# Kernel optimization log

Hardware: AMD Instinct MI355X
Metric: run time of the kernel (lower is better)

## Reference

```python
import jax, jax.numpy as jnp
import numpy as np
from jax import lax

NUM_HEADS = 4
DIM = 192
EPS = 1e-12  # torch F.normalize eps


def setup_inputs() -> dict:
    key = jax.random.key(0)
    ks = jax.random.split(key, 5)
    b, c, h, w = 8, DIM, 128, 128
    x = jax.random.normal(ks[0], (b, c, h, w), dtype=jnp.float32)
    f = jax.random.normal(ks[1], (b, c, h, w), dtype=jnp.float32)
    # conv weights, scaled like kaiming-ish init
    w_qkv = jax.random.normal(ks[2], (3 * c, c, 1, 1), dtype=jnp.float32) * (1.0 / np.sqrt(c))
    w_dw = jax.random.normal(ks[3], (3 * c, 1, 3, 3), dtype=jnp.float32) * (1.0 / 3.0)
    w_proj = jax.random.normal(ks[4], (c, c, 1, 1), dtype=jnp.float32) * (1.0 / np.sqrt(c))
    temperature = jnp.ones((NUM_HEADS, 1, 1), dtype=jnp.float32)
    return {"x": x, "f": f, "w_qkv": w_qkv, "w_dw": w_dw, "w_proj": w_proj,
            "temperature": temperature}


def _conv(x, w, groups=1):
    return lax.conv_general_dilated(
        x, w, window_strides=(1, 1), padding="SAME",
        dimension_numbers=("NCHW", "OIHW", "NCHW"),
        feature_group_count=groups)


def reference(x, f, w_qkv, w_dw, w_proj, temperature):
    b, c, h, w = x.shape
    x_in = x + f
    qkv = _conv(x_in, w_qkv)                 # [b, 3c, h, w] 1x1 conv
    qkv = _conv(qkv, w_dw, groups=3 * c)     # depthwise 3x3
    q, k, v = jnp.split(qkv, 3, axis=1)      # each [b, c, h, w]
    hw = h * w
    ch = c // NUM_HEADS

    def heads(t):
        return t.reshape(b, NUM_HEADS, ch, hw)  # 'b (head c) h w -> b head c (h w)'

    q, k, v = heads(q), heads(k), heads(v)
    # L2-normalize over spatial (last) dim, torch-style eps clamp
    q = q / jnp.maximum(jnp.linalg.norm(q, axis=-1, keepdims=True), EPS)
    k = k / jnp.maximum(jnp.linalg.norm(k, axis=-1, keepdims=True), EPS)
    # transposed (channel) attention: [b, head, ch, ch]
    attn = jnp.einsum("bhcn,bhdn->bhcd", q, k) * temperature[None]
    attn = jax.nn.softmax(attn, axis=-1)
    out = jnp.einsum("bhcd,bhdn->bhcn", attn, v)  # [b, head, ch, hw]
    out = out.reshape(b, c, h, w)
    return _conv(out, w_proj)
```

## Files before the change

### kernel.cpp

```cpp
#include <hip/hip_runtime.h>
#include <stdint.h>

#define NB 8
#define NC 192
#define NOC 576
#define NH 4
#define HW 16384
#define NCHUNK 16

typedef unsigned short u16;
typedef __bf16 v8bf __attribute__((ext_vector_type(8)));
typedef float v4f __attribute__((ext_vector_type(4)));
typedef u16 v8us __attribute__((ext_vector_type(8)));
typedef u16 v4us __attribute__((ext_vector_type(4)));

__device__ __forceinline__ u16 f2bf(float f) {
    uint32_t u = __float_as_uint(f);
    u += 0x7FFFu + ((u >> 16) & 1u);
    return (u16)(u >> 16);
}
__device__ __forceinline__ float bf2f(u16 u) {
    return __uint_as_float(((uint32_t)u) << 16);
}

__global__ void k_cvt_w(const float* __restrict__ w, u16* __restrict__ wb, int n) {
    int i = blockIdx.x * 256 + threadIdx.x;
    if (i < n) wb[i] = f2bf(w[i]);
}

__global__ __launch_bounds__(256, 2) void k_gemm_qkv(
    const float* __restrict__ x, const float* __restrict__ f,
    const u16* __restrict__ wb, u16* __restrict__ qkv, int b0)
{
    __shared__ u16 bt[64 * 192];
    const int t = threadIdx.x;
    const int bl = blockIdx.y;
    const int bg = b0 + bl;
    const int p0 = blockIdx.x * 64;

    {
        const int qp = t & 15;
        const int chw = t >> 4;
        const int px = qp * 4;
        #pragma unroll
        for (int pass = 0; pass < 12; ++pass) {
            const int ch = pass * 16 + chw;
            const size_t base = ((size_t)bg * NC + ch) * HW + p0 + px;
            const float4 xv = *reinterpret_cast<const float4*>(&x[base]);
            const float4 fv = *reinterpret_cast<const float4*>(&f[base]);
            const int c4 = ch >> 3, cl = ch & 7;
            bt[(px + 0) * 192 + ((c4 ^ ((px + 0) & 7)) << 3) + cl] = f2bf(xv.x + fv.x);
            bt[(px + 1) * 192 + ((c4 ^ ((px + 1) & 7)) << 3) + cl] = f2bf(xv.y + fv.y);
            bt[(px + 2) * 192 + ((c4 ^ ((px + 2) & 7)) << 3) + cl] = f2bf(xv.z + fv.z);
            bt[(px + 3) * 192 + ((c4 ^ ((px + 3) & 7)) << 3) + cl] = f2bf(xv.w + fv.w);
        }
    }
    __syncthreads();

    const int w = t >> 6, l = t & 63, lr = l & 15, lg = l >> 4;
    const int oc0 = w * 144;

    v4f acc[4][9];
    #pragma unroll
    for (int mi = 0; mi < 4; ++mi)
        #pragma unroll
        for (int ni = 0; ni < 9; ++ni)
            acc[mi][ni] = (v4f){0.f, 0.f, 0.f, 0.f};

    #pragma unroll
    for (int ks = 0; ks < 6; ++ks) {
        const int k = ks * 32 + lg * 8;
        const int c4 = ks * 4 + lg;
        v8bf a[4];
        #pragma unroll
        for (int mi = 0; mi < 4; ++mi) {
            const int px = mi * 16 + lr;
            a[mi] = *reinterpret_cast<const v8bf*>(&bt[px * 192 + ((c4 ^ (px & 7)) << 3)]);
        }
        #pragma unroll
        for (int ni = 0; ni < 9; ++ni) {
            const int oc = oc0 + ni * 16 + lr;
            const v8bf bw = *reinterpret_cast<const v8bf*>(&wb[oc * 192 + k]);
            #pragma unroll
            for (int mi = 0; mi < 4; ++mi)
                acc[mi][ni] = __builtin_amdgcn_mfma_f32_16x16x32_bf16(a[mi], bw, acc[mi][ni], 0, 0, 0);
        }
    }

    #pragma unroll
    for (int mi = 0; mi < 4; ++mi)
        #pragma unroll
        for (int ni = 0; ni < 9; ++ni) {
            const int oc = oc0 + ni * 16 + lr;
            const int px = p0 + mi * 16 + lg * 4;
            v4us pk;
            pk[0] = f2bf(acc[mi][ni][0]); pk[1] = f2bf(acc[mi][ni][1]);
            pk[2] = f2bf(acc[mi][ni][2]); pk[3] = f2bf(acc[mi][ni][3]);
            *reinterpret_cast<v4us*>(&qkv[((size_t)bl * NOC + oc) * HW + px]) = pk;
        }
}

__global__ __launch_bounds__(256) void k_dw(
    const u16* __restrict__ qkv, const float* __restrict__ wdw,
    u16* __restrict__ qk_out, u16* __restrict__ v_out,
    float* __restrict__ sumsq, int b0)
{
    __shared__ u16 plane[128 * 136];
    __shared__ float red[4];
    const int t = threadIdx.x;
    const int ch = blockIdx.x;
    const int bl = blockIdx.y;
    const int bg = b0 + bl;
    const size_t pbase = ((size_t)bl * NOC + ch) * HW;

    float wk[9];
    #pragma unroll
    for (int i = 0; i < 9; ++i) wk[i] = wdw[ch * 9 + i];

    const int r = t >> 1;
    const int cb = (t & 1) * 64;

    #pragma unroll
    for (int i = 0; i < 8; ++i) {
        v8us v = *reinterpret_cast<const v8us*>(&qkv[pbase + r * 128 + cb + i * 8]);
        *reinterpret_cast<v8us*>(&plane[r * 136 + cb + i * 8]) = v;
    }
    __syncthreads();

    const bool vm = (r > 0), vp = (r < 127);
    const u16* rowm = &plane[(r - 1) * 136];
    const u16* rowc = &plane[r * 136];
    const u16* rowp = &plane[(r + 1) * 136];

    float am, ac, bm, bc, cm, cc2;
    if (cb == 0) { am = 0.f; bm = 0.f; cm = 0.f; }
    else {
        am = vm ? bf2f(rowm[cb - 1]) : 0.f;
        bm = bf2f(rowc[cb - 1]);
        cm = vp ? bf2f(rowp[cb - 1]) : 0.f;
    }
    ac = vm ? bf2f(rowm[cb]) : 0.f;
    bc = bf2f(rowc[cb]);
    cc2 = vp ? bf2f(rowp[cb]) : 0.f;

    uint32_t ov[32];
    float ssq = 0.f;
    #pragma unroll
    for (int xp = 0; xp < 32; ++xp) {
        #pragma unroll
        for (int s2 = 0; s2 < 2; ++s2) {
            const int col = cb + xp * 2 + s2;
            float ap, bp, cp;
            if (col < 127) {
                ap = vm ? bf2f(rowm[col + 1]) : 0.f;
                bp = bf2f(rowc[col + 1]);
                cp = vp ? bf2f(rowp[col + 1]) : 0.f;
            } else { ap = 0.f; bp = 0.f; cp = 0.f; }
            float o = wk[0]*am + wk[1]*ac + wk[2]*ap
                    + wk[3]*bm + wk[4]*bc + wk[5]*bp
                    + wk[6]*cm + wk[7]*cc2 + wk[8]*cp;
            u16 ob = f2bf(o);
            float orr = bf2f(ob);
            ssq += orr * orr;
            ov[xp] = (s2 == 0) ? (uint32_t)ob : (ov[xp] | ((uint32_t)ob << 16));
            am = ac; ac = ap; bm = bc; bc = bp; cm = cc2; cc2 = cp;
        }
    }

    __syncthreads();
    #pragma unroll
    for (int i = 0; i < 32; ++i)
        *reinterpret_cast<uint32_t*>(&plane[r * 136 + cb + i * 2]) = ov[i];
    __syncthreads();

    u16* dst = (ch < 2 * NC) ? (qk_out + ((size_t)bg * (2 * NC) + ch) * HW)
                             : (v_out + ((size_t)bg * NC + (ch - 2 * NC)) * HW);
    #pragma unroll
    for (int i = 0; i < 8; ++i) {
        const int idx = i * 2048 + t * 8;
        const int rr = idx >> 7, cc = idx & 127;
        v8us v = *reinterpret_cast<const v8us*>(&plane[rr * 136 + cc]);
        *reinterpret_cast<v8us*>(&dst[idx]) = v;
    }

    #pragma unroll
    for (int off = 32; off > 0; off >>= 1) ssq += __shfl_down(ssq, off);
    if ((t & 63) == 0) red[t >> 6] = ssq;
    __syncthreads();
    if (t == 0 && ch < 2 * NC) sumsq[bg * (2 * NC) + ch] = red[0] + red[1] + red[2] + red[3];
}

__global__ __launch_bounds__(256) void k_attn(
    const u16* __restrict__ qk, float* __restrict__ partials)
{
    __shared__ float wsum[4 * 2304];
    const int t = threadIdx.x;
    const int chunk = blockIdx.x;
    const int h = blockIdx.y;
    const int b = blockIdx.z;
    const int w = t >> 6, l = t & 63, lr = l & 15, lg = l >> 4;

    const size_t qbase = ((size_t)b * 384 + h * 48) * HW;
    const size_t kbase = ((size_t)b * 384 + 192 + h * 48) * HW;
    const int pb = chunk * 1024 + w * 256;

    v4f acc[3][3];
    #pragma unroll
    for (int mi = 0; mi < 3; ++mi)
        #pragma unroll
        for (int ni = 0; ni < 3; ++ni)
            acc[mi][ni] = (v4f){0.f, 0.f, 0.f, 0.f};

    #pragma unroll
    for (int ks = 0; ks < 8; ++ks) {
        const int k = pb + ks * 32 + lg * 8;
        v8bf a[3], bb[3];
        #pragma unroll
        for (int mi = 0; mi < 3; ++mi)
            a[mi] = *reinterpret_cast<const v8bf*>(&qk[qbase + (size_t)(mi * 16 + lr) * HW + k]);
        #pragma unroll
        for (int ni = 0; ni < 3; ++ni)
            bb[ni] = *reinterpret_cast<const v8bf*>(&qk[kbase + (size_t)(ni * 16 + lr) * HW + k]);
        #pragma unroll
        for (int mi = 0; mi < 3; ++mi)
            #pragma unroll
            for (int ni = 0; ni < 3; ++ni)
                acc[mi][ni] = __builtin_amdgcn_mfma_f32_16x16x32_bf16(a[mi], bb[ni], acc[mi][ni], 0, 0, 0);
    }

    #pragma unroll
    for (int mi = 0; mi < 3; ++mi)
        #pragma unroll
        for (int ni = 0; ni < 3; ++ni)
            #pragma unroll
            for (int r = 0; r < 4; ++r)
                wsum[w * 2304 + (mi * 16 + lg * 4 + r) * 48 + ni * 16 + lr] = acc[mi][ni][r];
    __syncthreads();

    #pragma unroll
    for (int i = 0; i < 9; ++i) {
        const int e = t + i * 256;
        float s = wsum[e] + wsum[2304 + e] + wsum[4608 + e] + wsum[6912 + e];
        partials[(((size_t)(b * NH + h)) * NCHUNK + chunk) * 2304 + e] = s;
    }
}

__global__ __launch_bounds__(256) void k_smx(
    const float* __restrict__ partials, const float* __restrict__ sumsq,
    const float* __restrict__ wproj, const float* __restrict__ temp,
    u16* __restrict__ Mb)
{
    __shared__ float att[2304];
    __shared__ float rq[48], rk[48];
    const int t = threadIdx.x;
    const int h = blockIdx.x;
    const int b = blockIdx.y;

    if (t < 48) {
        float s = sumsq[b * 384 + h * 48 + t];
        rq[t] = 1.f / fmaxf(sqrtf(s), 1e-12f);
    } else if (t < 96) {
        float s = sumsq[b * 384 + 192 + h * 48 + (t - 48)];
        rk[t - 48] = 1.f / fmaxf(sqrtf(s), 1e-12f);
    }
    __syncthreads();
    const float tp = temp[h];
    #pragma unroll
    for (int i = 0; i < 9; ++i) {
        const int e = t + i * 256;
        const float* pp = &partials[(((size_t)(b * NH + h)) * NCHUNK) * 2304 + e];
        float s = 0.f;
        #pragma unroll
        for (int c = 0; c < NCHUNK; ++c) s += pp[(size_t)c * 2304];
        att[e] = s * rq[e / 48] * rk[e % 48] * tp;
    }
    __syncthreads();
    if (t < 48) {
        float m = -1e30f;
        #pragma unroll
        for (int j = 0; j < 48; ++j) m = fmaxf(m, att[t * 48 + j]);
        float s = 0.f;
        for (int j = 0; j < 48; ++j) { float e2 = __expf(att[t * 48 + j] - m); att[t * 48 + j] = e2; s += e2; }
        const float inv = 1.f / s;
        for (int j = 0; j < 48; ++j) att[t * 48 + j] *= inv;
    }
    __syncthreads();
    #pragma unroll
    for (int i = 0; i < 36; ++i) {
        const int idx = t + i * 256;
        const int oc = idx / 48, d = idx % 48;
        float s = 0.f;
        #pragma unroll
        for (int cc = 0; cc < 48; ++cc)
            s += wproj[oc * 192 + h * 48 + cc] * att[cc * 48 + d];
        Mb[((size_t)b * NC + oc) * NC + h * 48 + d] = f2bf(s);
    }
}

__global__ __launch_bounds__(256) void k_gemm_out(
    const u16* __restrict__ vp, const u16* __restrict__ Mb,
    float* __restrict__ out)
{
    __shared__ u16 bt[64 * 192];
    const int t = threadIdx.x;
    const int b = blockIdx.y;
    const int p0 = blockIdx.x * 64;

    {
        const int qp = t & 15;
        const int chw = t >> 4;
        const int px = qp * 4;
        #pragma unroll
        for (int pass = 0; pass < 12; ++pass) {
            const int ch = pass * 16 + chw;
            const v4us vv = *reinterpret_cast<const v4us*>(&vp[((size_t)b * NC + ch) * HW + p0 + px]);
            const int c4 = ch >> 3, cl = ch & 7;
            bt[(px + 0) * 192 + ((c4 ^ ((px + 0) & 7)) << 3) + cl] = vv[0];
            bt[(px + 1) * 192 + ((c4 ^ ((px + 1) & 7)) << 3) + cl] = vv[1];
            bt[(px + 2) * 192 + ((c4 ^ ((px + 2) & 7)) << 3) + cl] = vv[2];
            bt[(px + 3) * 192 + ((c4 ^ ((px + 3) & 7)) << 3) + cl] = vv[3];
        }
    }
    __syncthreads();

    const int w = t >> 6, l = t & 63, lr = l & 15, lg = l >> 4;
    const int oc0 = w * 48;

    v4f acc[4][3];
    #pragma unroll
    for (int mi = 0; mi < 4; ++mi)
        #pragma unroll
        for (int ni = 0; ni < 3; ++ni)
            acc[mi][ni] = (v4f){0.f, 0.f, 0.f, 0.f};

    #pragma unroll
    for (int ks = 0; ks < 6; ++ks) {
        const int k = ks * 32 + lg * 8;
        const int c4 = ks * 4 + lg;
        v8bf a[4];
        #pragma unroll
        for (int mi = 0; mi < 4; ++mi) {
            const int px = mi * 16 + lr;
            a[mi] = *reinterpret_cast<const v8bf*>(&bt[px * 192 + ((c4 ^ (px & 7)) << 3)]);
        }
        #pragma unroll
        for (int ni = 0; ni < 3; ++ni) {
            const int oc = oc0 + ni * 16 + lr;
            const v8bf bw = *reinterpret_cast<const v8bf*>(&Mb[((size_t)b * NC + oc) * NC + k]);
            #pragma unroll
            for (int mi = 0; mi < 4; ++mi)
                acc[mi][ni] = __builtin_amdgcn_mfma_f32_16x16x32_bf16(a[mi], bw, acc[mi][ni], 0, 0, 0);
        }
    }

    #pragma unroll
    for (int mi = 0; mi < 4; ++mi)
        #pragma unroll
        for (int ni = 0; ni < 3; ++ni) {
            const int oc = oc0 + ni * 16 + lr;
            const int px = p0 + mi * 16 + lg * 4;
            *reinterpret_cast<v4f*>(&out[((size_t)b * NC + oc) * HW + px]) = acc[mi][ni];
        }
}

extern "C" void kernel_launch(void* const* d_in, const int* in_sizes, int n_in,
                              void* d_out, int out_size, void* d_ws, size_t ws_size,
                              hipStream_t stream)
{
    (void)in_sizes; (void)n_in; (void)out_size;
    const float* x      = (const float*)d_in[0];
    const float* f      = (const float*)d_in[1];
    const float* w_qkv  = (const float*)d_in[2];
    const float* w_dw   = (const float*)d_in[3];
    const float* w_proj = (const float*)d_in[4];
    const float* temp   = (const float*)d_in[5];

    char* ws = (char*)d_ws;
    u16*   vws      = (u16*)(ws);
    u16*   wb       = (u16*)(ws + 50331648);
    float* sumsq    = (float*)(ws + 50552832);
    float* partials = (float*)(ws + 50565120);
    u16*   Mb       = (u16*)(ws + 55283712);
    const size_t FIXED = 55873536;
    const size_t PERB  = (size_t)NOC * HW * 2;
    u16*   qkv_raw  = (u16*)(ws + FIXED);

    int g = 1;
    if (ws_size > FIXED + PERB) {
        size_t avail = (ws_size - FIXED) / PERB;
        g = (int)(avail > 8 ? 8 : avail);
        if (g < 1) g = 1;
    }

    u16* qk_scratch = (u16*)d_out;
    float* out      = (float*)d_out;

    hipLaunchKernelGGL(k_cvt_w, dim3(432), dim3(256), 0, stream, w_qkv, wb, NOC * NC);
    for (int b0 = 0; b0 < NB; b0 += g) {
        const int nb = (b0 + g <= NB) ? g : (NB - b0);
        hipLaunchKernelGGL(k_gemm_qkv, dim3(HW / 64, nb), dim3(256), 0, stream, x, f, wb, qkv_raw, b0);
        hipLaunchKernelGGL(k_dw, dim3(NOC, nb), dim3(256), 0, stream, qkv_raw, w_dw, qk_scratch, vws, sumsq, b0);
    }
    hipLaunchKernelGGL(k_attn, dim3(NCHUNK, NH, NB), dim3(256), 0, stream, qk_scratch, partials);
    hipLaunchKernelGGL(k_smx, dim3(NH, NB), dim3(256), 0, stream, partials, sumsq, w_proj, temp, Mb);
    hipLaunchKernelGGL(k_gemm_out, dim3(HW / 64, NB), dim3(256), 0, stream, vws, Mb, out);
}
```

Measured before the change: 355.1 us.

## Stage QKV weights in LDS per k-step and vectorize transposed input staging

In the QKV GEMM, each 32-wide K slice of the bf16 weight matrix is now cooperatively loaded into a swizzled shared-memory tile before the MFMA loop, instead of every wave reading weights straight from global memory. The K loop is no longer unrolled and gains two barriers per step. Both GEMM kernels now gather 8 channels per pixel and write one 16-byte LDS store, instead of scattering individual 2-byte stores. The trade-off is lower global coalescing, since loads become scalar strided per channel, plus extra LDS usage (about 60KB) that may reduce occupancy.

```diff
diff --git a/kernel.cpp b/kernel.cpp
--- a/kernel.cpp
+++ b/kernel.cpp
@@ -33,29 +33,28 @@
     const u16* __restrict__ wb, u16* __restrict__ qkv, int b0)
 {
     __shared__ u16 bt[64 * 192];
+    __shared__ u16 wt[576 * 32];
     const int t = threadIdx.x;
     const int bl = blockIdx.y;
     const int bg = b0 + bl;
     const int p0 = blockIdx.x * 64;
 
     {
-        const int qp = t & 15;
-        const int chw = t >> 4;
-        const int px = qp * 4;
-        #pragma unroll
-        for (int pass = 0; pass < 12; ++pass) {
-            const int ch = pass * 16 + chw;
-            const size_t base = ((size_t)bg * NC + ch) * HW + p0 + px;
-            const float4 xv = *reinterpret_cast<const float4*>(&x[base]);
-            const float4 fv = *reinterpret_cast<const float4*>(&f[base]);
-            const int c4 = ch >> 3, cl = ch & 7;
-            bt[(px + 0) * 192 + ((c4 ^ ((px + 0) & 7)) << 3) + cl] = f2bf(xv.x + fv.x);
-            bt[(px + 1) * 192 + ((c4 ^ ((px + 1) & 7)) << 3) + cl] = f2bf(xv.y + fv.y);
-            bt[(px + 2) * 192 + ((c4 ^ ((px + 2) & 7)) << 3) + cl] = f2bf(xv.z + fv.z);
-            bt[(px + 3) * 192 + ((c4 ^ ((px + 3) & 7)) << 3) + cl] = f2bf(xv.w + fv.w);
-        }
-    }
-    __syncthreads();
+        const int px = t & 63;
+        const int cg = t >> 6;
+        #pragma unroll
+        for (int it = 0; it < 6; ++it) {
+            const int c4 = it * 4 + cg;
+            const size_t base = ((size_t)bg * NC + c4 * 8) * HW + p0 + px;
+            v8us pk;
+            #pragma unroll
+            for (int j = 0; j < 8; ++j) {
+                float v = x[base + (size_t)j * HW] + f[base + (size_t)j * HW];
+                pk[j] = f2bf(v);
+            }
+            *reinterpret_cast<v8us*>(&bt[px * 192 + ((c4 ^ (px & 7)) << 3)]) = pk;
+        }
+    }
 
     const int w = t >> 6, l = t & 63, lr = l & 15, lg = l >> 4;
     const int oc0 = w * 144;
@@ -67,20 +66,28 @@
         for (int ni = 0; ni < 9; ++ni)
             acc[mi][ni] = (v4f){0.f, 0.f, 0.f, 0.f};
 
-    #pragma unroll
+    #pragma unroll 1
     for (int ks = 0; ks < 6; ++ks) {
-        const int k = ks * 32 + lg * 8;
-        const int c4 = ks * 4 + lg;
+        __syncthreads();
+        #pragma unroll
+        for (int it = 0; it < 9; ++it) {
+            const int idx = it * 256 + t;
+            const int oc = idx >> 2, lgw = idx & 3;
+            v8us wv = *reinterpret_cast<const v8us*>(&wb[oc * 192 + ks * 32 + lgw * 8]);
+            *reinterpret_cast<v8us*>(&wt[oc * 32 + ((lgw ^ ((oc >> 1) & 3)) << 3)]) = wv;
+        }
+        __syncthreads();
+
         v8bf a[4];
         #pragma unroll
         for (int mi = 0; mi < 4; ++mi) {
             const int px = mi * 16 + lr;
-            a[mi] = *reinterpret_cast<const v8bf*>(&bt[px * 192 + ((c4 ^ (px & 7)) << 3)]);
+            a[mi] = *reinterpret_cast<const v8bf*>(&bt[px * 192 + (((ks * 4 + lg) ^ (px & 7)) << 3)]);
         }
         #pragma unroll
         for (int ni = 0; ni < 9; ++ni) {
             const int oc = oc0 + ni * 16 + lr;
-            const v8bf bw = *reinterpret_cast<const v8bf*>(&wb[oc * 192 + k]);
+            const v8bf bw = *reinterpret_cast<const v8bf*>(&wt[oc * 32 + ((lg ^ ((oc >> 1) & 3)) << 3)]);
             #pragma unroll
             for (int mi = 0; mi < 4; ++mi)
                 acc[mi][ni] = __builtin_amdgcn_mfma_f32_16x16x32_bf16(a[mi], bw, acc[mi][ni], 0, 0, 0);
@@ -307,18 +314,16 @@
     const int p0 = blockIdx.x * 64;
 
     {
-        const int qp = t & 15;
-        const int chw = t >> 4;
-        const int px = qp * 4;
-        #pragma unroll
-        for (int pass = 0; pass < 12; ++pass) {
-            const int ch = pass * 16 + chw;
-            const v4us vv = *reinterpret_cast<const v4us*>(&vp[((size_t)b * NC + ch) * HW + p0 + px]);
-            const int c4 = ch >> 3, cl = ch & 7;
-            bt[(px + 0) * 192 + ((c4 ^ ((px + 0) & 7)) << 3) + cl] = vv[0];
-            bt[(px + 1) * 192 + ((c4 ^ ((px + 1) & 7)) << 3) + cl] = vv[1];
-            bt[(px + 2) * 192 + ((c4 ^ ((px + 2) & 7)) << 3) + cl] = vv[2];
-            bt[(px + 3) * 192 + ((c4 ^ ((px + 3) & 7)) << 3) + cl] = vv[3];
+        const int px = t & 63;
+        const int cg = t >> 6;
+        #pragma unroll
+        for (int it = 0; it < 6; ++it) {
+            const int c4 = it * 4 + cg;
+            const size_t base = ((size_t)b * NC + c4 * 8) * HW + p0 + px;
+            v8us pk;
+            #pragma unroll
+            for (int j = 0; j < 8; ++j) pk[j] = vp[base + (size_t)j * HW];
+            *reinterpret_cast<v8us*>(&bt[px * 192 + ((c4 ^ (px & 7)) << 3)]) = pk;
         }
     }
     __syncthreads();
```

Result: faster. 333.5 us (-6.1%).
